# Optimization experiments

Measured on AMD Instinct MI355X. Metric: run time of the kernel, lower is better.

The kernel has to match this reference:

```python
import jax, jax.numpy as jnp
import numpy as np

N, F, E = 100000, 128, 1600000


def setup_inputs() -> dict:
    key = jax.random.key(0)
    ks = jax.random.split(key, 10)
    s = 1.0 / np.sqrt(F)
    return {
        "x": jax.random.normal(ks[0], (N, F), jnp.float32),
        "edge_index": jax.random.randint(ks[1], (2, E), 0, N),
        "edge_weight": jax.random.uniform(ks[2], (E,), jnp.float32),
        # EvolveGCNO initial weight (1, F, F) -> squeezed to (F, F)
        "initial_weight": jax.random.normal(ks[3], (F, F), jnp.float32) * s,
        # torch.nn.GRU(F, F) params, gate order (r, z, n)
        "gru_w_ih": jax.random.uniform(ks[4], (3 * F, F), jnp.float32, -s, s),
        "gru_w_hh": jax.random.uniform(ks[5], (3 * F, F), jnp.float32, -s, s),
        "gru_b_ih": jax.random.uniform(ks[6], (3 * F,), jnp.float32, -s, s),
        "gru_b_hh": jax.random.uniform(ks[7], (3 * F,), jnp.float32, -s, s),
        # Linear(F, 1)
        "lin_w": jax.random.uniform(ks[8], (1, F), jnp.float32, -s, s),
        "lin_b": jax.random.uniform(ks[9], (1,), jnp.float32, -s, s),
    }


def _evolve_weight(W0, w_ih, w_hh, b_ih, b_hh):
    # One GRU step: input = W0 rows (batch=F), hidden = W0 rows (first call of EvolveGCNO)
    gi = W0 @ w_ih.T + b_ih  # (F, 3F)
    gh = W0 @ w_hh.T + b_hh
    i_r, i_z, i_n = jnp.split(gi, 3, axis=-1)
    h_r, h_z, h_n = jnp.split(gh, 3, axis=-1)
    r = jax.nn.sigmoid(i_r + h_r)
    z = jax.nn.sigmoid(i_z + h_z)
    n = jnp.tanh(i_n + r * h_n)
    return (1.0 - z) * n + z * W0  # (F, F)


def reference(x, edge_index, edge_weight, initial_weight, gru_w_ih, gru_w_hh,
              gru_b_ih, gru_b_hh, lin_w, lin_b):
    W = _evolve_weight(initial_weight, gru_w_ih, gru_w_hh, gru_b_ih, gru_b_hh)
    n_nodes = x.shape[0]
    row, col = edge_index[0], edge_index[1]  # source, target
    # gcn_norm: add self loops (weight 1), sym-normalize D^-1/2 (A+I) D^-1/2
    loop = jnp.arange(n_nodes)
    row = jnp.concatenate([row, loop])
    col = jnp.concatenate([col, loop])
    w = jnp.concatenate([edge_weight, jnp.ones((n_nodes,), x.dtype)])
    deg = jax.ops.segment_sum(w, col, num_segments=n_nodes)
    dinv = jnp.where(deg > 0, jax.lax.rsqrt(deg), 0.0)
    norm = dinv[row] * w * dinv[col]  # (E+N,)
    xw = x @ W  # (N, F)
    # gather at sources, weighted scatter-add at targets
    h = jax.ops.segment_sum(norm[:, None] * xw[row], col, num_segments=n_nodes)
    h = jax.nn.relu(h)
    return (h @ lin_w.T + lin_b)[:, 0]  # (N,)
```

## Files before the change

### kernel.cpp

```cpp
#include <hip/hip_runtime.h>

#define F 128
#define DEG_SCALE 16777216.0f
#define DEG_INV   (1.0f / 16777216.0f)
#define BUCK_BITS 7
#define BUCK_COLS 128
#define CAP 2304
#define EPT 8
#define WB_STRIDE 136

typedef _Float16 half8 __attribute__((ext_vector_type(8)));
typedef float f32x4 __attribute__((ext_vector_type(4)));

__global__ __launch_bounds__(256) void init_kernel(
    int* __restrict__ cursor, int NZ, int NBUK,
    const float* __restrict__ W0, const float* __restrict__ wih,
    const float* __restrict__ whh, const float* __restrict__ bih,
    const float* __restrict__ bhh, float* __restrict__ W) {
  __shared__ float w0row[2][F];
  int b = blockIdx.x;
  if (b < NZ) {
    int i = b * 256 + threadIdx.x;
    if (i < NBUK) cursor[i] = 0;
    return;
  }
  int half = threadIdx.x >> 7;
  int j = threadIdx.x & 127;
  int i = (b - NZ) * 2 + half;
  w0row[half][j] = W0[i * F + j];
  __syncthreads();
  float ar = 0, az = 0, an = 0, br = 0, bz = 0, bn = 0;
  const float* wi_r = wih + (size_t)j * F;
  const float* wi_z = wih + (size_t)(j + F) * F;
  const float* wi_n = wih + (size_t)(j + 2 * F) * F;
  const float* wh_r = whh + (size_t)j * F;
  const float* wh_z = whh + (size_t)(j + F) * F;
  const float* wh_n = whh + (size_t)(j + 2 * F) * F;
#pragma unroll 4
  for (int k = 0; k < F; ++k) {
    float a = w0row[half][k];
    ar = fmaf(a, wi_r[k], ar);
    az = fmaf(a, wi_z[k], az);
    an = fmaf(a, wi_n[k], an);
    br = fmaf(a, wh_r[k], br);
    bz = fmaf(a, wh_z[k], bz);
    bn = fmaf(a, wh_n[k], bn);
  }
  float gr = ar + bih[j] + br + bhh[j];
  float gz = az + bih[j + F] + bz + bhh[j + F];
  float r = 1.f / (1.f + expf(-gr));
  float z = 1.f / (1.f + expf(-gz));
  float n = tanhf(an + bih[j + 2 * F] + r * (bn + bhh[j + 2 * F]));
  W[i * F + j] = (1.f - z) * n + z * w0row[half][j];
}

__global__ __launch_bounds__(1024) void bin_kernel(
    const int* __restrict__ row, const int* __restrict__ col,
    const float* __restrict__ ew, int* __restrict__ cursor,
    uint2* __restrict__ binned, int E, int NBUK) {
  __shared__ int cnt[1024];
  __shared__ int base[1024];
  int tid = threadIdx.x;
  cnt[tid] = 0;
  __syncthreads();
  int e0 = blockIdx.x * (1024 * EPT) + tid;
  int cc[EPT];
  int lrank[EPT];
#pragma unroll
  for (int k = 0; k < EPT; ++k) {
    int e = e0 + k * 1024;
    if (e < E) {
      cc[k] = col[e];
      lrank[k] = atomicAdd(&cnt[cc[k] >> BUCK_BITS], 1);
    } else cc[k] = -1;
  }
  __syncthreads();
  if (tid < NBUK) {
    int c = cnt[tid];
    base[tid] = c ? atomicAdd(&cursor[tid], c) : 0;
  }
  __syncthreads();
#pragma unroll
  for (int k = 0; k < EPT; ++k) {
    if (cc[k] >= 0) {
      int e = e0 + k * 1024;
      int b = cc[k] >> BUCK_BITS;
      int pos = base[b] + lrank[k];
      if (pos < CAP) {
        unsigned cl = (unsigned)(cc[k] & (BUCK_COLS - 1));
        binned[(size_t)b * CAP + pos] =
            make_uint2((unsigned)row[e] | (cl << 17), __float_as_uint(ew[e]));
      }
    }
  }
}

__global__ __launch_bounds__(256) void csr_kernel(
    const uint2* __restrict__ binned, const int* __restrict__ cursor,
    int* __restrict__ offs, float* __restrict__ dinv,
    uint2* __restrict__ pairs, int N, int NBUK) {
  __shared__ unsigned long long acc[BUCK_COLS];
  __shared__ float dinvL[BUCK_COLS];
  __shared__ int wbase[BUCK_COLS];
  __shared__ int sc[BUCK_COLS];
  __shared__ int wsum[4];
  int b = blockIdx.x;
  int tid = threadIdx.x;
  if (tid < BUCK_COLS) acc[tid] = 0ull;
  int partial = 0;
  for (int i = tid; i < b; i += 256) partial += cursor[i];
#pragma unroll
  for (int m = 32; m; m >>= 1) partial += __shfl_xor(partial, m);
  if ((tid & 63) == 0) wsum[tid >> 6] = partial;
  __syncthreads();
  int bstart = b * BUCK_COLS + wsum[0] + wsum[1] + wsum[2] + wsum[3];

  int cnt = cursor[b];
  if (cnt > CAP) cnt = CAP;
  const uint2* src = binned + (size_t)b * CAP;
  for (int i = tid; i < cnt; i += 256) {
    uint2 rec = src[i];
    int cl = rec.x >> 17;
    unsigned fx = (unsigned)(__uint_as_float(rec.y) * DEG_SCALE);
    atomicAdd(&acc[cl], ((unsigned long long)1 << 32) | (unsigned long long)fx);
  }
  __syncthreads();
  int node0 = b * BUCK_COLS;
  int cvt1 = 0;
  if (tid < BUCK_COLS) {
    unsigned long long pk = acc[tid];
    int node = node0 + tid;
    if (node < N) {
      cvt1 = (int)(pk >> 32) + 1;
      float deg = (float)(unsigned)(pk & 0xffffffffull) * DEG_INV;
      float dv = rsqrtf(deg + 1.0f);
      dinvL[tid] = dv;
      dinv[node] = dv;
    }
    sc[tid] = cvt1;
  }
  __syncthreads();
  for (int off = 1; off < BUCK_COLS; off <<= 1) {
    int x = 0;
    if (tid < BUCK_COLS && tid >= off) x = sc[tid - off];
    __syncthreads();
    if (tid < BUCK_COLS) sc[tid] += x;
    __syncthreads();
  }
  if (tid < BUCK_COLS) {
    int node = node0 + tid;
    if (node < N) {
      int abs0 = bstart + sc[tid] - cvt1;
      offs[node] = abs0;
      pairs[abs0] = make_uint2((unsigned)node << 8, __float_as_uint(dinvL[tid]));
      wbase[tid] = abs0 + 1;
    }
  }
  __syncthreads();
  for (int i = tid; i < cnt; i += 256) {
    uint2 rec = src[i];
    int cl = rec.x >> 17;
    unsigned r = rec.x & 0x1ffffu;
    float wp = __uint_as_float(rec.y) * dinvL[cl];
    int pos = atomicAdd(&wbase[cl], 1);
    pairs[pos] = make_uint2(r << 8, __float_as_uint(wp));
  }
}

__global__ __launch_bounds__(256) void norm_fix(
    uint2* __restrict__ pairs, const float* __restrict__ dinv,
    int* __restrict__ offs, int N, int total) {
  int i = blockIdx.x * 256 + threadIdx.x;
  if (i < total) {
    uint2 pr = pairs[i];
    float v = __uint_as_float(pr.y) * dinv[pr.x >> 8];
    pairs[i] = make_uint2(pr.x, __float_as_uint(v));
  } else if (i < total + 16) {
    pairs[i] = make_uint2(0u, 0u);
  }
  if (i == 0) offs[N] = total;
}

__global__ __launch_bounds__(256) void gemm_xw(
    const float* __restrict__ x, const float* __restrict__ W,
    _Float16* __restrict__ xwh, int N) {
  __shared__ _Float16 Wb[F * WB_STRIDE];
  int t = threadIdx.x;
  for (int idx = t; idx < F * F; idx += 256) {
    int k = idx >> 7, n = idx & 127;
    Wb[n * WB_STRIDE + k] = (_Float16)W[idx];
  }
  __syncthreads();

  int lane = t & 63, wave = t >> 6;
  int ln = lane & 15, q = lane >> 4;
  int rowb = blockIdx.x * 64 + wave * 16;
  int i = rowb + ln;
  int iclamp = (i < N) ? i : N - 1;
  const float* xp = x + (size_t)iclamp * F + q * 8;

  half8 a[4];
#pragma unroll
  for (int tt = 0; tt < 4; ++tt) {
    float4 v0 = *(const float4*)(xp + 32 * tt);
    float4 v1 = *(const float4*)(xp + 32 * tt + 4);
    half8 av;
    av[0] = (_Float16)v0.x; av[1] = (_Float16)v0.y;
    av[2] = (_Float16)v0.z; av[3] = (_Float16)v0.w;
    av[4] = (_Float16)v1.x; av[5] = (_Float16)v1.y;
    av[6] = (_Float16)v1.z; av[7] = (_Float16)v1.w;
    a[tt] = av;
  }

  f32x4 acc[8];
#pragma unroll
  for (int nt = 0; nt < 8; ++nt) acc[nt] = (f32x4){0.f, 0.f, 0.f, 0.f};

#pragma unroll
  for (int nt = 0; nt < 8; ++nt) {
#pragma unroll
    for (int tt = 0; tt < 4; ++tt) {
      half8 bfrag = *(const half8*)&Wb[(nt * 16 + ln) * WB_STRIDE + tt * 32 + q * 8];
      acc[nt] = __builtin_amdgcn_mfma_f32_16x16x32_f16(a[tt], bfrag, acc[nt], 0, 0, 0);
    }
  }

#pragma unroll
  for (int nt = 0; nt < 8; ++nt) {
#pragma unroll
    for (int r = 0; r < 4; ++r) {
      int rowi = rowb + q * 4 + r;
      if (rowi < N) xwh[(size_t)rowi * F + nt * 16 + ln] = (_Float16)acc[nt][r];
    }
  }
}

__global__ __launch_bounds__(256) void gather_out(
    const uint2* __restrict__ pairs, const int* __restrict__ offs,
    const char* __restrict__ xwb, const float* __restrict__ linw,
    const float* __restrict__ linb, float* __restrict__ out, int N) {
  int wave = threadIdx.x >> 6;
  int lane = threadIdx.x & 63;
  int node = blockIdx.x * 4 + wave;
  if (node >= N) return;
  int c = lane & 15;
  int q = lane >> 4;

  const char* xb = xwb + (c << 4);
  float acc[8];
#pragma unroll
  for (int j = 0; j < 8; ++j) acc[j] = 0.f;

  int start = offs[node], end = offs[node + 1];
  for (int it = start + q; it < end; it += 16) {
    uint2 p0 = pairs[it];
    uint2 p1 = pairs[it + 4];
    uint2 p2 = pairs[it + 8];
    uint2 p3 = pairs[it + 12];
    float n0 = __uint_as_float(p0.y);
    float n1 = (it + 4 < end) ? __uint_as_float(p1.y) : 0.f;
    float n2 = (it + 8 < end) ? __uint_as_float(p2.y) : 0.f;
    float n3 = (it + 12 < end) ? __uint_as_float(p3.y) : 0.f;
    half8 x0 = *(const half8*)(xb + p0.x);
    half8 x1 = *(const half8*)(xb + p1.x);
    half8 x2 = *(const half8*)(xb + p2.x);
    half8 x3 = *(const half8*)(xb + p3.x);
#pragma unroll
    for (int j = 0; j < 8; ++j) acc[j] = fmaf(n0, (float)x0[j], acc[j]);
#pragma unroll
    for (int j = 0; j < 8; ++j) acc[j] = fmaf(n1, (float)x1[j], acc[j]);
#pragma unroll
    for (int j = 0; j < 8; ++j) acc[j] = fmaf(n2, (float)x2[j], acc[j]);
#pragma unroll
    for (int j = 0; j < 8; ++j) acc[j] = fmaf(n3, (float)x3[j], acc[j]);
  }

#pragma unroll
  for (int j = 0; j < 8; ++j) {
    acc[j] += __shfl_xor(acc[j], 16);
    acc[j] += __shfl_xor(acc[j], 32);
  }

  const float4* lw4 = (const float4*)linw;
  float4 la = lw4[c * 2];
  float4 lb = lw4[c * 2 + 1];
  float p = fmaxf(acc[0], 0.f) * la.x + fmaxf(acc[1], 0.f) * la.y +
            fmaxf(acc[2], 0.f) * la.z + fmaxf(acc[3], 0.f) * la.w +
            fmaxf(acc[4], 0.f) * lb.x + fmaxf(acc[5], 0.f) * lb.y +
            fmaxf(acc[6], 0.f) * lb.z + fmaxf(acc[7], 0.f) * lb.w;
#pragma unroll
  for (int m = 8; m; m >>= 1) p += __shfl_xor(p, m);

  if (lane == 0) out[node] = p + linb[0];
}

extern "C" void kernel_launch(void* const* d_in, const int* in_sizes, int n_in,
                              void* d_out, int out_size, void* d_ws, size_t ws_size,
                              hipStream_t stream) {
  const float* x    = (const float*)d_in[0];
  const int*   ei   = (const int*)d_in[1];
  const float* ew   = (const float*)d_in[2];
  const float* W0   = (const float*)d_in[3];
  const float* wih  = (const float*)d_in[4];
  const float* whh  = (const float*)d_in[5];
  const float* bih  = (const float*)d_in[6];
  const float* bhh  = (const float*)d_in[7];
  const float* linw = (const float*)d_in[8];
  const float* linb = (const float*)d_in[9];

  int N = in_sizes[0] / F;
  int E = in_sizes[2];
  const int* row = ei;
  const int* col = ei + E;
  int NBUK = (N + BUCK_COLS - 1) / BUCK_COLS;
  int total = E + N;

  char* p = (char*)d_ws;
  auto alloc = [&](size_t bytes) {
    char* q = p;
    p += (bytes + 255) & ~(size_t)255;
    return q;
  };
  float*    W      = (float*)alloc((size_t)F * F * 4);
  int*      cursor = (int*)alloc((size_t)NBUK * 4);
  float*    dinv   = (float*)alloc((size_t)N * 4);
  int*      offs   = (int*)alloc(((size_t)N + 1) * 4);
  uint2*    binned = (uint2*)alloc((size_t)NBUK * CAP * 8);
  uint2*    pairs  = (uint2*)alloc(((size_t)total + 16) * 8);
  _Float16* xwh    = (_Float16*)alloc((size_t)N * F * 2);

  int NZ = (NBUK + 255) / 256;
  init_kernel<<<NZ + 64, 256, 0, stream>>>(cursor, NZ, NBUK, W0, wih, whh, bih, bhh, W);

  int EPB = 1024 * EPT;
  bin_kernel<<<(E + EPB - 1) / EPB, 1024, 0, stream>>>(row, col, ew, cursor, binned,
                                                       E, NBUK);
  csr_kernel<<<NBUK, 256, 0, stream>>>(binned, cursor, offs, dinv, pairs, N, NBUK);
  norm_fix<<<(total + 16 + 255) / 256, 256, 0, stream>>>(pairs, dinv, offs, N, total);

  gemm_xw<<<(N + 63) / 64, 256, 0, stream>>>(x, W, xwh, N);
  gather_out<<<(N + 3) / 4, 256, 0, stream>>>(pairs, offs, (const char*)xwh,
                                              linw, linb, (float*)d_out, N);
}
```

Before: 255.4 us.

## Fuse GEMM with edge binning, drop norm_fix, sort CSR in LDS, apply dinv in gather

The x@W GEMM and the edge binning now run in one launch, with blocks split by index (1024-thread blocks, 256 rows per GEMM block). The separate norm_fix pass is removed: the source-side dinv factor is now looked up per edge inside gather_out. csr_kernel sorts each bucket in shared memory and writes it to global in one contiguous pass. Gather loads for the tail of each edge group are now predicated instead of reading padding. The cost is an extra random dinv load per edge in the gather and a larger LDS footprint in csr_kernel, which can lower its occupancy.

```diff
diff --git a/kernel.cpp b/kernel.cpp
--- a/kernel.cpp
+++ b/kernel.cpp
@@ -54,139 +54,54 @@
   W[i * F + j] = (1.f - z) * n + z * w0row[half][j];
 }
 
-__global__ __launch_bounds__(1024) void bin_kernel(
+__global__ __launch_bounds__(1024) void gemm_bin(
+    const float* __restrict__ x, const float* __restrict__ W,
+    _Float16* __restrict__ xwh, int N, int GB,
     const int* __restrict__ row, const int* __restrict__ col,
     const float* __restrict__ ew, int* __restrict__ cursor,
     uint2* __restrict__ binned, int E, int NBUK) {
+  __shared__ _Float16 Wb[F * WB_STRIDE];
   __shared__ int cnt[1024];
   __shared__ int base[1024];
-  int tid = threadIdx.x;
-  cnt[tid] = 0;
-  __syncthreads();
-  int e0 = blockIdx.x * (1024 * EPT) + tid;
-  int cc[EPT];
-  int lrank[EPT];
-#pragma unroll
-  for (int k = 0; k < EPT; ++k) {
-    int e = e0 + k * 1024;
-    if (e < E) {
-      cc[k] = col[e];
-      lrank[k] = atomicAdd(&cnt[cc[k] >> BUCK_BITS], 1);
-    } else cc[k] = -1;
-  }
-  __syncthreads();
-  if (tid < NBUK) {
-    int c = cnt[tid];
-    base[tid] = c ? atomicAdd(&cursor[tid], c) : 0;
-  }
-  __syncthreads();
-#pragma unroll
-  for (int k = 0; k < EPT; ++k) {
-    if (cc[k] >= 0) {
+  int t = threadIdx.x;
+
+  if ((int)blockIdx.x >= GB) {
+    cnt[t] = 0;
+    __syncthreads();
+    int e0 = ((int)blockIdx.x - GB) * (1024 * EPT) + t;
+    int cc[EPT];
+    int lrank[EPT];
+#pragma unroll
+    for (int k = 0; k < EPT; ++k) {
       int e = e0 + k * 1024;
-      int b = cc[k] >> BUCK_BITS;
-      int pos = base[b] + lrank[k];
-      if (pos < CAP) {
-        unsigned cl = (unsigned)(cc[k] & (BUCK_COLS - 1));
-        binned[(size_t)b * CAP + pos] =
-            make_uint2((unsigned)row[e] | (cl << 17), __float_as_uint(ew[e]));
+      if (e < E) {
+        cc[k] = col[e];
+        lrank[k] = atomicAdd(&cnt[cc[k] >> BUCK_BITS], 1);
+      } else cc[k] = -1;
+    }
+    __syncthreads();
+    if (t < NBUK) {
+      int c = cnt[t];
+      base[t] = c ? atomicAdd(&cursor[t], c) : 0;
+    }
+    __syncthreads();
+#pragma unroll
+    for (int k = 0; k < EPT; ++k) {
+      if (cc[k] >= 0) {
+        int e = e0 + k * 1024;
+        int b = cc[k] >> BUCK_BITS;
+        int pos = base[b] + lrank[k];
+        if (pos < CAP) {
+          unsigned cl = (unsigned)(cc[k] & (BUCK_COLS - 1));
+          binned[(size_t)b * CAP + pos] =
+              make_uint2((unsigned)row[e] | (cl << 17), __float_as_uint(ew[e]));
+        }
       }
     }
-  }
-}
-
-__global__ __launch_bounds__(256) void csr_kernel(
-    const uint2* __restrict__ binned, const int* __restrict__ cursor,
-    int* __restrict__ offs, float* __restrict__ dinv,
-    uint2* __restrict__ pairs, int N, int NBUK) {
-  __shared__ unsigned long long acc[BUCK_COLS];
-  __shared__ float dinvL[BUCK_COLS];
-  __shared__ int wbase[BUCK_COLS];
-  __shared__ int sc[BUCK_COLS];
-  __shared__ int wsum[4];
-  int b = blockIdx.x;
-  int tid = threadIdx.x;
-  if (tid < BUCK_COLS) acc[tid] = 0ull;
-  int partial = 0;
-  for (int i = tid; i < b; i += 256) partial += cursor[i];
-#pragma unroll
-  for (int m = 32; m; m >>= 1) partial += __shfl_xor(partial, m);
-  if ((tid & 63) == 0) wsum[tid >> 6] = partial;
-  __syncthreads();
-  int bstart = b * BUCK_COLS + wsum[0] + wsum[1] + wsum[2] + wsum[3];
-
-  int cnt = cursor[b];
-  if (cnt > CAP) cnt = CAP;
-  const uint2* src = binned + (size_t)b * CAP;
-  for (int i = tid; i < cnt; i += 256) {
-    uint2 rec = src[i];
-    int cl = rec.x >> 17;
-    unsigned fx = (unsigned)(__uint_as_float(rec.y) * DEG_SCALE);
-    atomicAdd(&acc[cl], ((unsigned long long)1 << 32) | (unsigned long long)fx);
-  }
-  __syncthreads();
-  int node0 = b * BUCK_COLS;
-  int cvt1 = 0;
-  if (tid < BUCK_COLS) {
-    unsigned long long pk = acc[tid];
-    int node = node0 + tid;
-    if (node < N) {
-      cvt1 = (int)(pk >> 32) + 1;
-      float deg = (float)(unsigned)(pk & 0xffffffffull) * DEG_INV;
-      float dv = rsqrtf(deg + 1.0f);
-      dinvL[tid] = dv;
-      dinv[node] = dv;
-    }
-    sc[tid] = cvt1;
-  }
-  __syncthreads();
-  for (int off = 1; off < BUCK_COLS; off <<= 1) {
-    int x = 0;
-    if (tid < BUCK_COLS && tid >= off) x = sc[tid - off];
-    __syncthreads();
-    if (tid < BUCK_COLS) sc[tid] += x;
-    __syncthreads();
-  }
-  if (tid < BUCK_COLS) {
-    int node = node0 + tid;
-    if (node < N) {
-      int abs0 = bstart + sc[tid] - cvt1;
-      offs[node] = abs0;
-      pairs[abs0] = make_uint2((unsigned)node << 8, __float_as_uint(dinvL[tid]));
-      wbase[tid] = abs0 + 1;
-    }
-  }
-  __syncthreads();
-  for (int i = tid; i < cnt; i += 256) {
-    uint2 rec = src[i];
-    int cl = rec.x >> 17;
-    unsigned r = rec.x & 0x1ffffu;
-    float wp = __uint_as_float(rec.y) * dinvL[cl];
-    int pos = atomicAdd(&wbase[cl], 1);
-    pairs[pos] = make_uint2(r << 8, __float_as_uint(wp));
-  }
-}
-
-__global__ __launch_bounds__(256) void norm_fix(
-    uint2* __restrict__ pairs, const float* __restrict__ dinv,
-    int* __restrict__ offs, int N, int total) {
-  int i = blockIdx.x * 256 + threadIdx.x;
-  if (i < total) {
-    uint2 pr = pairs[i];
-    float v = __uint_as_float(pr.y) * dinv[pr.x >> 8];
-    pairs[i] = make_uint2(pr.x, __float_as_uint(v));
-  } else if (i < total + 16) {
-    pairs[i] = make_uint2(0u, 0u);
-  }
-  if (i == 0) offs[N] = total;
-}
-
-__global__ __launch_bounds__(256) void gemm_xw(
-    const float* __restrict__ x, const float* __restrict__ W,
-    _Float16* __restrict__ xwh, int N) {
-  __shared__ _Float16 Wb[F * WB_STRIDE];
-  int t = threadIdx.x;
-  for (int idx = t; idx < F * F; idx += 256) {
+    return;
+  }
+
+  for (int idx = t; idx < F * F; idx += 1024) {
     int k = idx >> 7, n = idx & 127;
     Wb[n * WB_STRIDE + k] = (_Float16)W[idx];
   }
@@ -194,7 +109,7 @@
 
   int lane = t & 63, wave = t >> 6;
   int ln = lane & 15, q = lane >> 4;
-  int rowb = blockIdx.x * 64 + wave * 16;
+  int rowb = blockIdx.x * 256 + wave * 16;
   int i = rowb + ln;
   int iclamp = (i < N) ? i : N - 1;
   const float* xp = x + (size_t)iclamp * F + q * 8;
@@ -235,10 +150,88 @@
   }
 }
 
+__global__ __launch_bounds__(256) void csr_kernel(
+    const uint2* __restrict__ binned, const int* __restrict__ cursor,
+    int* __restrict__ offs, float* __restrict__ dinv,
+    uint2* __restrict__ pairs, int N, int NBUK) {
+  __shared__ unsigned long long acc[BUCK_COLS];
+  __shared__ float dinvL[BUCK_COLS];
+  __shared__ int sc[BUCK_COLS];
+  __shared__ int woff[BUCK_COLS];
+  __shared__ int wsum[4];
+  __shared__ uint2 sorted[CAP + BUCK_COLS];
+  int b = blockIdx.x;
+  int tid = threadIdx.x;
+  if (tid < BUCK_COLS) acc[tid] = 0ull;
+  int partial = 0;
+  for (int i = tid; i < b; i += 256) partial += cursor[i];
+#pragma unroll
+  for (int m = 32; m; m >>= 1) partial += __shfl_xor(partial, m);
+  if ((tid & 63) == 0) wsum[tid >> 6] = partial;
+  __syncthreads();
+  int bstart = b * BUCK_COLS + wsum[0] + wsum[1] + wsum[2] + wsum[3];
+
+  int cnt = cursor[b];
+  if (cnt > CAP) cnt = CAP;
+  const uint2* src = binned + (size_t)b * CAP;
+  for (int i = tid; i < cnt; i += 256) {
+    uint2 rec = src[i];
+    int cl = rec.x >> 17;
+    unsigned fx = (unsigned)(__uint_as_float(rec.y) * DEG_SCALE);
+    atomicAdd(&acc[cl], ((unsigned long long)1 << 32) | (unsigned long long)fx);
+  }
+  __syncthreads();
+  int node0 = b * BUCK_COLS;
+  int cvt1 = 0;
+  if (tid < BUCK_COLS) {
+    int node = node0 + tid;
+    if (node < N) {
+      unsigned long long pk = acc[tid];
+      cvt1 = (int)(pk >> 32) + 1;
+      float deg = (float)(unsigned)(pk & 0xffffffffull) * DEG_INV;
+      float dv = rsqrtf(deg + 1.0f);
+      dinvL[tid] = dv;
+      dinv[node] = dv;
+    }
+    sc[tid] = cvt1;
+  }
+  __syncthreads();
+  for (int off = 1; off < BUCK_COLS; off <<= 1) {
+    int x = 0;
+    if (tid < BUCK_COLS && tid >= off) x = sc[tid - off];
+    __syncthreads();
+    if (tid < BUCK_COLS) sc[tid] += x;
+    __syncthreads();
+  }
+  if (tid < BUCK_COLS) {
+    int node = node0 + tid;
+    if (node < N) {
+      int rel0 = sc[tid] - cvt1;
+      offs[node] = bstart + rel0;
+      sorted[rel0] = make_uint2((unsigned)node << 8, __float_as_uint(dinvL[tid]));
+      woff[tid] = rel0 + 1;
+    }
+  }
+  __syncthreads();
+  for (int i = tid; i < cnt; i += 256) {
+    uint2 rec = src[i];
+    int cl = rec.x >> 17;
+    unsigned r = rec.x & 0x1ffffu;
+    float wp = __uint_as_float(rec.y) * dinvL[cl];
+    int pos = atomicAdd(&woff[cl], 1);
+    sorted[pos] = make_uint2(r << 8, __float_as_uint(wp));
+  }
+  __syncthreads();
+  int tot = sc[BUCK_COLS - 1];
+  for (int i = tid; i < tot; i += 256) pairs[bstart + i] = sorted[i];
+  if (b == NBUK - 1 && tid == 0) offs[N] = bstart + tot;
+}
+
 __global__ __launch_bounds__(256) void gather_out(
     const uint2* __restrict__ pairs, const int* __restrict__ offs,
-    const char* __restrict__ xwb, const float* __restrict__ linw,
-    const float* __restrict__ linb, float* __restrict__ out, int N) {
+    const float* __restrict__ dinv, const char* __restrict__ xwb,
+    const float* __restrict__ linw, const float* __restrict__ linb,
+    float* __restrict__ out, int N) {
   int wave = threadIdx.x >> 6;
   int lane = threadIdx.x & 63;
   int node = blockIdx.x * 4 + wave;
@@ -251,20 +244,36 @@
 #pragma unroll
   for (int j = 0; j < 8; ++j) acc[j] = 0.f;
 
+  half8 zero8 = {0, 0, 0, 0, 0, 0, 0, 0};
+  uint2 p1 = make_uint2(0u, 0u), p2 = p1, p3 = p1;
+  half8 x1 = zero8, x2 = zero8, x3 = zero8;
+  float d1 = 0.f, d2 = 0.f, d3 = 0.f;
+
   int start = offs[node], end = offs[node + 1];
   for (int it = start + q; it < end; it += 16) {
     uint2 p0 = pairs[it];
-    uint2 p1 = pairs[it + 4];
-    uint2 p2 = pairs[it + 8];
-    uint2 p3 = pairs[it + 12];
-    float n0 = __uint_as_float(p0.y);
-    float n1 = (it + 4 < end) ? __uint_as_float(p1.y) : 0.f;
-    float n2 = (it + 8 < end) ? __uint_as_float(p2.y) : 0.f;
-    float n3 = (it + 12 < end) ? __uint_as_float(p3.y) : 0.f;
     half8 x0 = *(const half8*)(xb + p0.x);
-    half8 x1 = *(const half8*)(xb + p1.x);
-    half8 x2 = *(const half8*)(xb + p2.x);
-    half8 x3 = *(const half8*)(xb + p3.x);
+    float d0 = dinv[p0.x >> 8];
+    bool v1 = it + 4 < end, v2 = it + 8 < end, v3 = it + 12 < end;
+    if (v1) {
+      p1 = pairs[it + 4];
+      x1 = *(const half8*)(xb + p1.x);
+      d1 = dinv[p1.x >> 8];
+    }
+    if (v2) {
+      p2 = pairs[it + 8];
+      x2 = *(const half8*)(xb + p2.x);
+      d2 = dinv[p2.x >> 8];
+    }
+    if (v3) {
+      p3 = pairs[it + 12];
+      x3 = *(const half8*)(xb + p3.x);
+      d3 = dinv[p3.x >> 8];
+    }
+    float n0 = __uint_as_float(p0.y) * d0;
+    float n1 = v1 ? __uint_as_float(p1.y) * d1 : 0.f;
+    float n2 = v2 ? __uint_as_float(p2.y) * d2 : 0.f;
+    float n3 = v3 ? __uint_as_float(p3.y) * d3 : 0.f;
 #pragma unroll
     for (int j = 0; j < 8; ++j) acc[j] = fmaf(n0, (float)x0[j], acc[j]);
 #pragma unroll
@@ -326,19 +335,19 @@
   float*    dinv   = (float*)alloc((size_t)N * 4);
   int*      offs   = (int*)alloc(((size_t)N + 1) * 4);
   uint2*    binned = (uint2*)alloc((size_t)NBUK * CAP * 8);
-  uint2*    pairs  = (uint2*)alloc(((size_t)total + 16) * 8);
+  uint2*    pairs  = (uint2*)alloc((size_t)total * 8);
   _Float16* xwh    = (_Float16*)alloc((size_t)N * F * 2);
 
   int NZ = (NBUK + 255) / 256;
   init_kernel<<<NZ + 64, 256, 0, stream>>>(cursor, NZ, NBUK, W0, wih, whh, bih, bhh, W);
 
-  int EPB = 1024 * EPT;
-  bin_kernel<<<(E + EPB - 1) / EPB, 1024, 0, stream>>>(row, col, ew, cursor, binned,
-                                                       E, NBUK);
+  int GB = (N + 255) / 256;
+  int BB = (E + 1024 * EPT - 1) / (1024 * EPT);
+  gemm_bin<<<GB + BB, 1024, 0, stream>>>(x, W, xwh, N, GB,
+                                         row, col, ew, cursor, binned, E, NBUK);
+
   csr_kernel<<<NBUK, 256, 0, stream>>>(binned, cursor, offs, dinv, pairs, N, NBUK);
-  norm_fix<<<(total + 16 + 255) / 256, 256, 0, stream>>>(pairs, dinv, offs, N, total);
-
-  gemm_xw<<<(N + 63) / 64, 256, 0, stream>>>(x, W, xwh, N);
-  gather_out<<<(N + 3) / 4, 256, 0, stream>>>(pairs, offs, (const char*)xwh,
+
+  gather_out<<<(N + 3) / 4, 256, 0, stream>>>(pairs, offs, dinv, (const char*)xwh,
                                               linw, linb, (float*)d_out, N);
 }
```

Result: no change. 257.0 us (+0.6%).
